# Kernel optimization log

Measured on AMD Instinct MI355X. Metric: run time of the kernel, lower is better.

Reference implementation:

```python
import jax, jax.numpy as jnp
import numpy as np

DIM = 1024
DEPTH = 6
HEADS = 8
FF_MULT = 4
LN_EPS = 1e-5
LEAKY_SLOPE = 0.01


def _layernorm(x, w, b):
    m = jnp.mean(x, axis=-1, keepdims=True)
    v = jnp.mean(jnp.square(x - m), axis=-1, keepdims=True)
    return (x - m) * jax.lax.rsqrt(v + LN_EPS) * w + b


def setup_inputs() -> dict:
    key = jax.random.key(0)
    ks = jax.random.split(key, 12)
    b, t = 2, 4096
    s = 0.02  # weight init scale
    return {
        "x": jax.random.normal(ks[0], (b, t, DIM), dtype=jnp.float32),
        "ln1_w": jnp.ones((DEPTH, DIM), jnp.float32),
        "ln1_b": jnp.zeros((DEPTH, DIM), jnp.float32),
        "wq": jax.random.normal(ks[1], (DEPTH, DIM, DIM), jnp.float32) * s,
        "wk": jax.random.normal(ks[2], (DEPTH, DIM, DIM), jnp.float32) * s,
        "wv": jax.random.normal(ks[3], (DEPTH, DIM, DIM), jnp.float32) * s,
        "wo": jax.random.normal(ks[4], (DEPTH, DIM, DIM), jnp.float32) * s,
        "bo": jnp.zeros((DEPTH, DIM), jnp.float32),
        "ln2_w": jnp.ones((DEPTH, DIM), jnp.float32),
        "ln2_b": jnp.zeros((DEPTH, DIM), jnp.float32),
        "w1": jax.random.normal(ks[5], (DEPTH, DIM, FF_MULT * DIM), jnp.float32) * s,
        "w2": jax.random.normal(ks[6], (DEPTH, FF_MULT * DIM, DIM), jnp.float32) * s,
    }


def _linear_attn(q, k, v):
    # q,k,v: [b,h,n,d]; non-causal kernelized linear attention
    q = jax.nn.softmax(q, axis=-1)        # over feature dim d
    k = jax.nn.softmax(k, axis=-2)        # over sequence dim n
    context = jnp.einsum('bhnd,bhne->bhde', k, v)
    return jnp.einsum('bhnd,bhde->bhne', q, context)


def reference(x, ln1_w, ln1_b, wq, wk, wv, wo, bo, ln2_w, ln2_b, w1, w2):
    b, t, e = x.shape
    h, dh = HEADS, e // HEADS
    for i in range(DEPTH):
        # PreNorm + SelfAttention + residual
        xn = _layernorm(x, ln1_w[i], ln1_b[i])
        q = (xn @ wq[i]).reshape(b, t, h, dh).transpose(0, 2, 1, 3)
        k = (xn @ wk[i]).reshape(b, t, h, dh).transpose(0, 2, 1, 3)
        v = (xn @ wv[i]).reshape(b, t, h, dh).transpose(0, 2, 1, 3)
        attn = _linear_attn(q, k, v)                      # [b,h,t,dh]
        attn = attn.transpose(0, 2, 1, 3).reshape(b, t, e)
        x = attn @ wo[i] + bo[i] + x
        # PreNorm + FeedForward + residual
        xn = _layernorm(x, ln2_w[i], ln2_b[i])
        hdn = xn @ w1[i]
        hdn = jnp.where(hdn >= 0, hdn, LEAKY_SLOPE * hdn)  # LeakyReLU(0.01)
        x = hdn @ w2[i] + x
    return x
```

## Files before the change

kernel.cpp:

```cpp
#include <hip/hip_runtime.h>

typedef unsigned short u16;
typedef unsigned int u32;
typedef unsigned long long uptr;

typedef __bf16 bf16x8 __attribute__((ext_vector_type(8)));
typedef float f32x4 __attribute__((ext_vector_type(4)));
typedef u16 u16x8 __attribute__((ext_vector_type(8)));
typedef u16 u16x4 __attribute__((ext_vector_type(4)));
typedef u16 u16x2 __attribute__((ext_vector_type(2)));

static __device__ __forceinline__ u16 f2bf(float f) {
    u32 x = __float_as_uint(f);
    u32 r = x + 0x7fffu + ((x >> 16) & 1u);
    return (u16)(r >> 16);
}
static __device__ __forceinline__ float bf2f(u16 u) {
    return __uint_as_float(((u32)u) << 16);
}

static __device__ __forceinline__ void async_cp16(const u16* g, const u16* lds) {
    __builtin_amdgcn_global_load_lds(
        (__attribute__((address_space(1))) u32*)(uptr)(const void*)g,
        (__attribute__((address_space(3))) u32*)(u32)(uptr)(const void*)lds,
        16, 0, 0);
}

enum { E_F32 = 0, E_BF16 = 1, E_BIASRES = 2, E_LEAKY = 3, E_RES = 4, E_VT = 5, E_EXPT = 6 };

template <int EPI>
__global__ __launch_bounds__(256, 2) void gemm_tn(
    const u16* __restrict__ A, const u16* __restrict__ B, void* __restrict__ C,
    const float* __restrict__ bias, const float* __restrict__ res,
    float* __restrict__ colsum,
    int K, int lda, int ldb, int ldc, int H, int ZS,
    long sAb, long sAh, long sBb, long sBh, long sCb, long sCh, long sCz)
{
    constexpr bool TRANSOUT = (EPI == E_VT || EPI == E_EXPT);
    __shared__ u16 smem[TRANSOUT ? 17408 : 8192];

    const int tid  = threadIdx.x;
    const int lane = tid & 63;
    const int wid  = tid >> 6;
    const int wm   = (wid >> 1) * 64;
    const int wn   = (wid & 1) * 64;
    const int m0   = blockIdx.y * 128;
    const int n0   = blockIdx.x * 128;
    const int z    = blockIdx.z;
    const int bb   = z / (H * ZS);
    const int hh   = (z / ZS) % H;
    const int zsp  = z % ZS;

    const u16* Ab = A + bb * sAb + hh * sAh + (long)zsp * K;
    const u16* Bb = B + bb * sBb + hh * sBh + (long)zsp * K;

    const int srow = wid * 32 + (lane >> 2);
    const int skel = (lane & 3) * 8;
    const u16* aS = Ab + (long)(m0 + srow) * lda + skel;
    const u16* bS = Bb + (long)(n0 + srow) * ldb + skel;

    const int aoff = (wm + (lane & 15)) * 32 + (lane >> 4) * 8;
    const int boff = 4096 + (wn + (lane & 15)) * 32 + (lane >> 4) * 8;

    f32x4 acc[4][4] = {};

    const int nk = K >> 5;
    for (int kt = 0; kt < nk; ++kt) {
        __syncthreads();
        const u16* a0 = aS + kt * 32;
        const u16* b0 = bS + kt * 32;
        async_cp16(a0,            smem + wid * 1024);
        async_cp16(a0 + 16 * lda, smem + wid * 1024 + 512);
        async_cp16(b0,            smem + 4096 + wid * 1024);
        async_cp16(b0 + 16 * ldb, smem + 4096 + wid * 1024 + 512);
        __syncthreads();

        bf16x8 af[4], bfg[4];
#pragma unroll
        for (int i = 0; i < 4; ++i) af[i]  = *(const bf16x8*)(smem + aoff + i * 512);
#pragma unroll
        for (int i = 0; i < 4; ++i) bfg[i] = *(const bf16x8*)(smem + boff + i * 512);
#pragma unroll
        for (int mi = 0; mi < 4; ++mi)
#pragma unroll
            for (int ni = 0; ni < 4; ++ni)
                acc[mi][ni] = __builtin_amdgcn_mfma_f32_16x16x32_bf16(af[mi], bfg[ni], acc[mi][ni], 0, 0, 0);
    }

    const int r0 = (lane >> 4) * 4;
    const int cc = lane & 15;

    if constexpr (EPI == E_F32 || EPI == E_BIASRES || EPI == E_RES) {
        float* Cf = (float*)C + bb * sCb + hh * sCh + (long)zsp * sCz;
#pragma unroll
        for (int mi = 0; mi < 4; ++mi)
#pragma unroll
            for (int ni = 0; ni < 4; ++ni) {
                const int col = n0 + wn + ni * 16 + cc;
#pragma unroll
                for (int r = 0; r < 4; ++r) {
                    const int row = m0 + wm + mi * 16 + r0 + r;
                    float v = acc[mi][ni][r];
                    if constexpr (EPI == E_BIASRES) v += bias[col] + res[(long)row * ldc + col];
                    if constexpr (EPI == E_RES)     v += res[(long)row * ldc + col];
                    Cf[(long)row * ldc + col] = v;
                }
            }
    } else if constexpr (EPI == E_BF16 || EPI == E_LEAKY) {
        u16* Cb = (u16*)C + bb * sCb + hh * sCh;
#pragma unroll
        for (int mi = 0; mi < 4; ++mi)
#pragma unroll
            for (int ni = 0; ni < 4; ++ni) {
                const int col = n0 + wn + ni * 16 + cc;
#pragma unroll
                for (int r = 0; r < 4; ++r) {
                    const int row = m0 + wm + mi * 16 + r0 + r;
                    float v = acc[mi][ni][r];
                    if constexpr (EPI == E_LEAKY) v = (v >= 0.f) ? v : 0.01f * v;
                    Cb[(long)row * ldc + col] = f2bf(v);
                }
            }
    } else {
        __syncthreads();
#pragma unroll
        for (int mi = 0; mi < 4; ++mi)
#pragma unroll
            for (int ni = 0; ni < 4; ++ni)
#pragma unroll
                for (int r = 0; r < 4; ++r) {
                    float v = acc[mi][ni][r];
                    if constexpr (EPI == E_EXPT) v = __expf(v);
                    smem[(wn + ni * 16 + cc) * 136 + wm + mi * 16 + r0 + r] = f2bf(v);
                }
        __syncthreads();
        const int c = tid >> 1, hf = tid & 1;
        const u16* srcp = smem + c * 136 + hf * 64;
        const long base = ((long)(m0 >> 12) * 1024 + n0 + c) * 4096 + (m0 & 4095) + hf * 64;
        u16* Ob = (u16*)C;
        float s = 0.f;
#pragma unroll
        for (int j = 0; j < 8; ++j) {
            u16x8 vv = *(const u16x8*)(srcp + j * 8);
            if constexpr (EPI == E_EXPT) {
#pragma unroll
                for (int q = 0; q < 8; ++q) s += bf2f(vv[q]);
            }
            *(u16x8*)(Ob + base + j * 8) = vv;
        }
        if constexpr (EPI == E_EXPT) {
            s += __shfl_xor(s, 1);
            if (hf == 0) atomicAdd(&colsum[(m0 >> 12) * 1024 + n0 + c], s);
        }
    }
}

__global__ __launch_bounds__(256) void layernorm_k(
    const float* __restrict__ x, const float* __restrict__ w,
    const float* __restrict__ b, u16* __restrict__ out)
{
    const int row = blockIdx.x, tid = threadIdx.x, lane = tid & 63, wid = tid >> 6;
    float4 v = ((const float4*)x)[row * 256 + tid];
    float s  = v.x + v.y + v.z + v.w;
    float ss = v.x * v.x + v.y * v.y + v.z * v.z + v.w * v.w;
#pragma unroll
    for (int o = 32; o >= 1; o >>= 1) { s += __shfl_xor(s, o); ss += __shfl_xor(ss, o); }
    __shared__ float red[8];
    if (lane == 0) { red[wid] = s; red[4 + wid] = ss; }
    __syncthreads();
    s  = red[0] + red[1] + red[2] + red[3];
    ss = red[4] + red[5] + red[6] + red[7];
    const float mean = s * (1.f / 1024.f);
    const float var  = ss * (1.f / 1024.f) - mean * mean;
    const float rs   = rsqrtf(var + 1e-5f);
    float4 wv = ((const float4*)w)[tid];
    float4 bv = ((const float4*)b)[tid];
    u16x4 o;
    o[0] = f2bf((v.x - mean) * rs * wv.x + bv.x);
    o[1] = f2bf((v.y - mean) * rs * wv.y + bv.y);
    o[2] = f2bf((v.z - mean) * rs * wv.z + bv.z);
    o[3] = f2bf((v.w - mean) * rs * wv.w + bv.w);
    *(u16x4*)(out + (long)row * 1024 + tid * 4) = o;
}

__global__ __launch_bounds__(256) void qsoftmax_k(u16* __restrict__ q)
{
    const int tid = threadIdx.x, lane = tid & 63, wid = tid >> 6;
    const long seg = (long)blockIdx.x * 4 + wid;
    u16* p = q + seg * 128;
    u16x2 raw = *(const u16x2*)(p + lane * 2);
    float a = bf2f(raw[0]), b = bf2f(raw[1]);
    float m = fmaxf(a, b);
#pragma unroll
    for (int o = 32; o >= 1; o >>= 1) m = fmaxf(m, __shfl_xor(m, o));
    float e0 = __expf(a - m), e1 = __expf(b - m);
    float s = e0 + e1;
#pragma unroll
    for (int o = 32; o >= 1; o >>= 1) s += __shfl_xor(s, o);
    const float inv = 1.f / s;
    u16x2 o2; o2[0] = f2bf(e0 * inv); o2[1] = f2bf(e1 * inv);
    *(u16x2*)(p + lane * 2) = o2;
}

__global__ __launch_bounds__(256) void ctxreduce_k(
    const float* __restrict__ part, const float* __restrict__ S, u16* __restrict__ ctxb)
{
    const int idx = blockIdx.x * 256 + threadIdx.x;
    const int bh = idx >> 14;
    const int d  = idx & 127;
    float s = 0.f;
#pragma unroll
    for (int ks = 0; ks < 16; ++ks) s += part[(long)(bh * 16 + ks) * 16384 + (idx & 16383)];
    s /= S[(bh >> 3) * 1024 + (bh & 7) * 128 + d];
    ctxb[idx] = f2bf(s);
}

__global__ __launch_bounds__(256) void transw_k(
    const float* __restrict__ in, u16* __restrict__ out, int R, int C)
{
    __shared__ u16 t[64 * 68];
    const long moff = (long)blockIdx.z * R * C;
    const float* inp = in + moff;
    u16* outp = out + moff;
    const int r0 = blockIdx.y * 64, c0 = blockIdx.x * 64;
    const int tid = threadIdx.x;
    const int rr = tid >> 4, c4 = (tid & 15) * 4;
#pragma unroll
    for (int i = 0; i < 4; ++i) {
        const int r = rr + i * 16;
        float4 v = *(const float4*)(inp + (long)(r0 + r) * C + c0 + c4);
        u16x4 h; h[0] = f2bf(v.x); h[1] = f2bf(v.y); h[2] = f2bf(v.z); h[3] = f2bf(v.w);
        *(u16x4*)(t + r * 68 + c4) = h;
    }
    __syncthreads();
    const int c = tid >> 2, rs = (tid & 3) * 16;
    u16x8 o0, o1;
#pragma unroll
    for (int i = 0; i < 8; ++i) o0[i] = t[(rs + i) * 68 + c];
#pragma unroll
    for (int i = 0; i < 8; ++i) o1[i] = t[(rs + 8 + i) * 68 + c];
    u16* dst = outp + (long)(c0 + c) * R + r0 + rs;
    *(u16x8*)dst = o0;
    *(u16x8*)(dst + 8) = o1;
}

extern "C" void kernel_launch(void* const* d_in, const int* in_sizes, int n_in,
                              void* d_out, int out_size, void* d_ws, size_t ws_size,
                              hipStream_t stream)
{
    const float* x0   = (const float*)d_in[0];
    const float* ln1w = (const float*)d_in[1];
    const float* ln1b = (const float*)d_in[2];
    const float* wq   = (const float*)d_in[3];
    const float* wk   = (const float*)d_in[4];
    const float* wv   = (const float*)d_in[5];
    const float* wo   = (const float*)d_in[6];
    const float* bo   = (const float*)d_in[7];
    const float* ln2w = (const float*)d_in[8];
    const float* ln2b = (const float*)d_in[9];
    const float* w1   = (const float*)d_in[10];
    const float* w2   = (const float*)d_in[11];
    float* xout = (float*)d_out;

    char* ws = (char*)d_ws;
    size_t off = 0;
    auto alloc = [&](size_t bytes) -> void* {
        void* p = ws + off;
        off += (bytes + 255) & ~(size_t)255;
        return p;
    };
    u16* wqt   = (u16*)alloc(6ull * 1024 * 1024 * 2);
    u16* wkt   = (u16*)alloc(6ull * 1024 * 1024 * 2);
    u16* wvt   = (u16*)alloc(6ull * 1024 * 1024 * 2);
    u16* wot   = (u16*)alloc(6ull * 1024 * 1024 * 2);
    u16* w1t   = (u16*)alloc(6ull * 1024 * 4096 * 2);
    u16* w2t   = (u16*)alloc(6ull * 4096 * 1024 * 2);
    u16* xn    = (u16*)alloc(8192ull * 1024 * 2);
    u16* qb    = (u16*)alloc(8192ull * 1024 * 2);
    u16* kt    = (u16*)alloc(8192ull * 1024 * 2);
    u16* vt    = (u16*)alloc(8192ull * 1024 * 2);
    u16* attnb = (u16*)alloc(8192ull * 1024 * 2);
    u16* hdn   = (u16*)alloc(8192ull * 4096 * 2);
    float* part = (float*)alloc(256ull * 16384 * 4);
    u16* ctxb  = (u16*)alloc(262144ull * 2);
    float* Ssum = (float*)alloc(8192);

    const dim3 blk(256);

    transw_k<<<dim3(16, 16, 6), blk, 0, stream>>>(wq, wqt, 1024, 1024);
    transw_k<<<dim3(16, 16, 6), blk, 0, stream>>>(wk, wkt, 1024, 1024);
    transw_k<<<dim3(16, 16, 6), blk, 0, stream>>>(wv, wvt, 1024, 1024);
    transw_k<<<dim3(16, 16, 6), blk, 0, stream>>>(wo, wot, 1024, 1024);
    transw_k<<<dim3(64, 16, 6), blk, 0, stream>>>(w1, w1t, 1024, 4096);
    transw_k<<<dim3(16, 64, 6), blk, 0, stream>>>(w2, w2t, 4096, 1024);

    for (int L = 0; L < 6; ++L) {
        const float* xin = (L == 0) ? x0 : xout;

        layernorm_k<<<8192, blk, 0, stream>>>(xin, ln1w + L * 1024, ln1b + L * 1024, xn);

        gemm_tn<E_BF16><<<dim3(8, 64, 1), blk, 0, stream>>>(
            xn, wqt + (size_t)L * 1048576, qb, nullptr, nullptr, nullptr,
            1024, 1024, 1024, 1024, 1, 1, 0, 0, 0, 0, 0, 0, 0);

        hipMemsetAsync(Ssum, 0, 8192, stream);

        gemm_tn<E_EXPT><<<dim3(8, 64, 1), blk, 0, stream>>>(
            xn, wkt + (size_t)L * 1048576, kt, nullptr, nullptr, Ssum,
            1024, 1024, 1024, 0, 1, 1, 0, 0, 0, 0, 0, 0, 0);

        gemm_tn<E_VT><<<dim3(8, 64, 1), blk, 0, stream>>>(
            xn, wvt + (size_t)L * 1048576, vt, nullptr, nullptr, nullptr,
            1024, 1024, 1024, 0, 1, 1, 0, 0, 0, 0, 0, 0, 0);

        qsoftmax_k<<<16384, blk, 0, stream>>>(qb);

        gemm_tn<E_F32><<<dim3(1, 1, 256), blk, 0, stream>>>(
            vt, kt, part, nullptr, nullptr, nullptr,
            256, 4096, 4096, 128, 8, 16,
            4194304L, 524288L, 4194304L, 524288L, 2097152L, 262144L, 16384L);

        ctxreduce_k<<<1024, blk, 0, stream>>>(part, Ssum, ctxb);

        gemm_tn<E_BF16><<<dim3(1, 32, 16), blk, 0, stream>>>(
            qb, ctxb, attnb, nullptr, nullptr, nullptr,
            128, 1024, 128, 1024, 8, 1,
            4194304L, 128L, 131072L, 16384L, 4194304L, 128L, 0L);

        gemm_tn<E_BIASRES><<<dim3(8, 64, 1), blk, 0, stream>>>(
            attnb, wot + (size_t)L * 1048576, xout, bo + L * 1024, xin, nullptr,
            1024, 1024, 1024, 1024, 1, 1, 0, 0, 0, 0, 0, 0, 0);

        layernorm_k<<<8192, blk, 0, stream>>>(xout, ln2w + L * 1024, ln2b + L * 1024, xn);

        gemm_tn<E_LEAKY><<<dim3(32, 64, 1), blk, 0, stream>>>(
            xn, w1t + (size_t)L * 4194304, hdn, nullptr, nullptr, nullptr,
            1024, 1024, 1024, 4096, 1, 1, 0, 0, 0, 0, 0, 0, 0);

        gemm_tn<E_RES><<<dim3(8, 64, 1), blk, 0, stream>>>(
            hdn, w2t + (size_t)L * 4194304, xout, nullptr, xout, nullptr,
            4096, 4096, 4096, 1024, 1, 1, 0, 0, 0, 0, 0, 0, 0);
    }
}
```

Before: 2.777 ms.

## Fuse Q/K/V projections into one GEMM and add XCD-aware block swizzle

Packs the transposed Q, K and V weights into one concatenated matrix per layer. A single GEMM launch now covers all three projections, and each block picks its epilogue by column range: row-major bf16 for Q, and transposed output for K (with exp and column-sum) and for V. It also remaps block indices so that consecutive work-groups are spread across the 8 chiplets (XCDs) when the grid size is a multiple of 8, which changes which tiles share an L2. This removes two launches and rereads of the normalized input, at the cost of a larger grid with mixed epilogues and a shared-memory size chosen for the worst case.

Result: faster. 2.482 ms (-10.6%).

```diff
diff --git a/kernel.cpp b/kernel.cpp
--- a/kernel.cpp
+++ b/kernel.cpp
@@ -26,26 +26,35 @@
         16, 0, 0);
 }
 
-enum { E_F32 = 0, E_BF16 = 1, E_BIASRES = 2, E_LEAKY = 3, E_RES = 4, E_VT = 5, E_EXPT = 6 };
+enum { E_F32 = 0, E_BF16 = 1, E_BIASRES = 2, E_LEAKY = 3, E_RES = 4, E_QKV = 5 };
 
 template <int EPI>
 __global__ __launch_bounds__(256, 2) void gemm_tn(
     const u16* __restrict__ A, const u16* __restrict__ B, void* __restrict__ C,
+    void* __restrict__ C2, void* __restrict__ C3,
     const float* __restrict__ bias, const float* __restrict__ res,
     float* __restrict__ colsum,
     int K, int lda, int ldb, int ldc, int H, int ZS,
     long sAb, long sAh, long sBb, long sBh, long sCb, long sCh, long sCz)
 {
-    constexpr bool TRANSOUT = (EPI == E_VT || EPI == E_EXPT);
-    __shared__ u16 smem[TRANSOUT ? 17408 : 8192];
+    __shared__ u16 smem[EPI == E_QKV ? 17408 : 8192];
 
     const int tid  = threadIdx.x;
     const int lane = tid & 63;
     const int wid  = tid >> 6;
     const int wm   = (wid >> 1) * 64;
     const int wn   = (wid & 1) * 64;
-    const int m0   = blockIdx.y * 128;
-    const int n0   = blockIdx.x * 128;
+
+    const int gx = gridDim.x;
+    int lin = blockIdx.x + gx * blockIdx.y;
+    const int nwg = gx * gridDim.y;
+    if ((nwg & 7) == 0) {
+        const int q8 = nwg >> 3;
+        lin = (lin & 7) * q8 + (lin >> 3);
+    }
+    const int n0 = (lin % gx) * 128;
+    const int m0 = (lin / gx) * 128;
+
     const int z    = blockIdx.z;
     const int bb   = z / (H * ZS);
     const int hh   = (z / ZS) % H;
@@ -121,36 +130,53 @@
                     Cb[(long)row * ldc + col] = f2bf(v);
                 }
             }
-    } else {
-        __syncthreads();
-#pragma unroll
-        for (int mi = 0; mi < 4; ++mi)
-#pragma unroll
-            for (int ni = 0; ni < 4; ++ni)
-#pragma unroll
-                for (int r = 0; r < 4; ++r) {
-                    float v = acc[mi][ni][r];
-                    if constexpr (EPI == E_EXPT) v = __expf(v);
-                    smem[(wn + ni * 16 + cc) * 136 + wm + mi * 16 + r0 + r] = f2bf(v);
+    } else if constexpr (EPI == E_QKV) {
+        if (n0 < 1024) {
+            u16* Cb = (u16*)C;
+#pragma unroll
+            for (int mi = 0; mi < 4; ++mi)
+#pragma unroll
+                for (int ni = 0; ni < 4; ++ni) {
+                    const int col = n0 + wn + ni * 16 + cc;
+#pragma unroll
+                    for (int r = 0; r < 4; ++r) {
+                        const int row = m0 + wm + mi * 16 + r0 + r;
+                        Cb[(long)row * ldc + col] = f2bf(acc[mi][ni][r]);
+                    }
                 }
-        __syncthreads();
-        const int c = tid >> 1, hf = tid & 1;
-        const u16* srcp = smem + c * 136 + hf * 64;
-        const long base = ((long)(m0 >> 12) * 1024 + n0 + c) * 4096 + (m0 & 4095) + hf * 64;
-        u16* Ob = (u16*)C;
-        float s = 0.f;
-#pragma unroll
-        for (int j = 0; j < 8; ++j) {
-            u16x8 vv = *(const u16x8*)(srcp + j * 8);
-            if constexpr (EPI == E_EXPT) {
-#pragma unroll
-                for (int q = 0; q < 8; ++q) s += bf2f(vv[q]);
+        } else {
+            const bool isK = (n0 < 2048);
+            const int nb = n0 - (isK ? 1024 : 2048);
+            __syncthreads();
+#pragma unroll
+            for (int mi = 0; mi < 4; ++mi)
+#pragma unroll
+                for (int ni = 0; ni < 4; ++ni)
+#pragma unroll
+                    for (int r = 0; r < 4; ++r) {
+                        float v = acc[mi][ni][r];
+                        if (isK) v = __expf(v);
+                        smem[(wn + ni * 16 + cc) * 136 + wm + mi * 16 + r0 + r] = f2bf(v);
+                    }
+            __syncthreads();
+            const int c = tid >> 1, hf = tid & 1;
+            const u16* srcp = smem + c * 136 + hf * 64;
+            const long base = ((long)(m0 >> 12) * 1024 + nb + c) * 4096 + (m0 & 4095) + hf * 64;
+            u16* Ob = (u16*)(isK ? C2 : C3);
+            float s = 0.f;
+#pragma unroll
+            for (int j = 0; j < 8; ++j) {
+                u16x8 vv = *(const u16x8*)(srcp + j * 8);
+                if (isK) {
+#pragma unroll
+                    for (int qq = 0; qq < 8; ++qq) s += bf2f(vv[qq]);
+                }
+                *(u16x8*)(Ob + base + j * 8) = vv;
             }
-            *(u16x8*)(Ob + base + j * 8) = vv;
-        }
-        if constexpr (EPI == E_EXPT) {
-            s += __shfl_xor(s, 1);
-            if (hf == 0) atomicAdd(&colsum[(m0 >> 12) * 1024 + n0 + c], s);
+            if (isK) {
+                s += __shfl_xor(s, 1);
+                if (hf == 0) atomicAdd(&colsum[(m0 >> 12) * 1024 + nb + c], s);
+            }
         }
     }
 }
@@ -216,12 +242,12 @@
 }
 
 __global__ __launch_bounds__(256) void transw_k(
-    const float* __restrict__ in, u16* __restrict__ out, int R, int C)
+    const float* __restrict__ in, u16* __restrict__ out, int R, int C,
+    long inZ, long outZ)
 {
     __shared__ u16 t[64 * 68];
-    const long moff = (long)blockIdx.z * R * C;
-    const float* inp = in + moff;
-    u16* outp = out + moff;
+    const float* inp = in + (long)blockIdx.z * inZ;
+    u16* outp = out + (long)blockIdx.z * outZ;
     const int r0 = blockIdx.y * 64, c0 = blockIdx.x * 64;
     const int tid = threadIdx.x;
     const int rr = tid >> 4, c4 = (tid & 15) * 4;
@@ -269,9 +295,7 @@
         off += (bytes + 255) & ~(size_t)255;
         return p;
     };
-    u16* wqt   = (u16*)alloc(6ull * 1024 * 1024 * 2);
-    u16* wkt   = (u16*)alloc(6ull * 1024 * 1024 * 2);
-    u16* wvt   = (u16*)alloc(6ull * 1024 * 1024 * 2);
+    u16* wqkvt = (u16*)alloc(6ull * 3072 * 1024 * 2);
     u16* wot   = (u16*)alloc(6ull * 1024 * 1024 * 2);
     u16* w1t   = (u16*)alloc(6ull * 1024 * 4096 * 2);
     u16* w2t   = (u16*)alloc(6ull * 4096 * 1024 * 2);
@@ -287,58 +311,52 @@
 
     const dim3 blk(256);
 
-    transw_k<<<dim3(16, 16, 6), blk, 0, stream>>>(wq, wqt, 1024, 1024);
-    transw_k<<<dim3(16, 16, 6), blk, 0, stream>>>(wk, wkt, 1024, 1024);
-    transw_k<<<dim3(16, 16, 6), blk, 0, stream>>>(wv, wvt, 1024, 1024);
-    transw_k<<<dim3(16, 16, 6), blk, 0, stream>>>(wo, wot, 1024, 1024);
-    transw_k<<<dim3(64, 16, 6), blk, 0, stream>>>(w1, w1t, 1024, 4096);
-    transw_k<<<dim3(16, 64, 6), blk, 0, stream>>>(w2, w2t, 4096, 1024);
+    transw_k<<<dim3(16, 16, 6), blk, 0, stream>>>(wq, wqkvt,           1024, 1024, 1048576L, 3145728L);
+    transw_k<<<dim3(16, 16, 6), blk, 0, stream>>>(wk, wqkvt + 1048576, 1024, 1024, 1048576L, 3145728L);
+    transw_k<<<dim3(16, 16, 6), blk, 0, stream>>>(wv, wqkvt + 2097152, 1024, 1024, 1048576L, 3145728L);
+    transw_k<<<dim3(16, 16, 6), blk, 0, stream>>>(wo, wot, 1024, 1024, 1048576L, 1048576L);
+    transw_k<<<dim3(64, 16, 6), blk, 0, stream>>>(w1, w1t, 1024, 4096, 4194304L, 4194304L);
+    transw_k<<<dim3(16, 64, 6), blk, 0, stream>>>(w2, w2t, 4096, 1024, 4194304L, 4194304L);
 
     for (int L = 0; L < 6; ++L) {
         const float* xin = (L == 0) ? x0 : xout;
 
         layernorm_k<<<8192, blk, 0, stream>>>(xin, ln1w + L * 1024, ln1b + L * 1024, xn);
 
-        gemm_tn<E_BF16><<<dim3(8, 64, 1), blk, 0, stream>>>(
-            xn, wqt + (size_t)L * 1048576, qb, nullptr, nullptr, nullptr,
+        hipMemsetAsync(Ssum, 0, 8192, stream);
+
+        gemm_tn<E_QKV><<<dim3(24, 64, 1), blk, 0, stream>>>(
+            xn, wqkvt + (size_t)L * 3145728, qb, kt, vt, nullptr, nullptr, Ssum,
             1024, 1024, 1024, 1024, 1, 1, 0, 0, 0, 0, 0, 0, 0);
 
-        hipMemsetAsync(Ssum, 0, 8192, stream);
-
-        gemm_tn<E_EXPT><<<dim3(8, 64, 1), blk, 0, stream>>>(
-            xn, wkt + (size_t)L * 1048576, kt, nullptr, nullptr, Ssum,
-            1024, 1024, 1024, 0, 1, 1, 0, 0, 0, 0, 0, 0, 0);
-
-        gemm_tn<E_VT><<<dim3(8, 64, 1), blk, 0, stream>>>(
-            xn, wvt + (size_t)L * 1048576, vt, nullptr, nullptr, nullptr,
-            1024, 1024, 1024, 0, 1, 1, 0, 0, 0, 0, 0, 0, 0);
-
         qsoftmax_k<<<16384, blk, 0, stream>>>(qb);
 
         gemm_tn<E_F32><<<dim3(1, 1, 256), blk, 0, stream>>>(
-            vt, kt, part, nullptr, nullptr, nullptr,
+            vt, kt, part, nullptr, nullptr, nullptr, nullptr, nullptr,
             256, 4096, 4096, 128, 8, 16,
             4194304L, 524288L, 4194304L, 524288L, 2097152L, 262144L, 16384L);
 
         ctxreduce_k<<<1024, blk, 0, stream>>>(part, Ssum, ctxb);
 
         gemm_tn<E_BF16><<<dim3(1, 32, 16), blk, 0, stream>>>(
-            qb, ctxb, attnb, nullptr, nullptr, nullptr,
+            qb, ctxb, attnb, nullptr, nullptr, nullptr, nullptr, nullptr,
             128, 1024, 128, 1024, 8, 1,
             4194304L, 128L, 131072L, 16384L, 4194304L, 128L, 0L);
 
         gemm_tn<E_BIASRES><<<dim3(8, 64, 1), blk, 0, stream>>>(
-            attnb, wot + (size_t)L * 1048576, xout, bo + L * 1024, xin, nullptr,
+            attnb, wot + (size_t)L * 1048576, xout, nullptr, nullptr,
+            bo + L * 1024, xin, nullptr,
             1024, 1024, 1024, 1024, 1, 1, 0, 0, 0, 0, 0, 0, 0);
 
         layernorm_k<<<8192, blk, 0, stream>>>(xout, ln2w + L * 1024, ln2b + L * 1024, xn);
 
         gemm_tn<E_LEAKY><<<dim3(32, 64, 1), blk, 0, stream>>>(
-            xn, w1t + (size_t)L * 4194304, hdn, nullptr, nullptr, nullptr,
+            xn, w1t + (size_t)L * 4194304, hdn, nullptr, nullptr, nullptr, nullptr, nullptr,
             1024, 1024, 1024, 4096, 1, 1, 0, 0, 0, 0, 0, 0, 0);
 
         gemm_tn<E_RES><<<dim3(8, 64, 1), blk, 0, stream>>>(
-            hdn, w2t + (size_t)L * 4194304, xout, nullptr, xout, nullptr,
+            hdn, w2t + (size_t)L * 4194304, xout, nullptr, nullptr,
+            nullptr, xout, nullptr,
             4096, 4096, 4096, 1024, 1, 1, 0, 0, 0, 0, 0, 0, 0);
     }
 }
```
